# Kernel optimization log

Hardware: AMD Instinct MI355X
Metric: run time of the kernel (lower is better)

The kernel has to match this reference:

```python
import jax, jax.numpy as jnp
import numpy as np

N, DIN, DOUT = 8192, 128, 128
NEG = -9.0e15  # the module's -9000000000000000.0 mask value
ALPHA = 0.2    # LeakyReLU negative slope


def setup_inputs() -> dict:
    key = jax.random.key(0)
    kx, ka, kw, ks, kr = jax.random.split(key, 5)
    X = jax.random.normal(kx, (N, DIN), dtype=jnp.float32)
    A = (jax.random.uniform(ka, (N, N)) < 0.01).astype(jnp.float32)
    A = A.at[jnp.arange(N), jnp.arange(N)].set(1.0)
    # Linear weight (Kaiming-uniform-ish range is irrelevant to math; use Xavier)
    lim_w = float(np.sqrt(6.0 / (DIN + DOUT)))
    W = jax.random.uniform(kw, (DOUT, DIN), jnp.float32, -lim_w, lim_w)
    b = jnp.zeros((DOUT,), jnp.float32)
    lim_a = float(np.sqrt(6.0 / (DOUT + 1)))
    a_s = jax.random.uniform(ks, (DOUT, 1), jnp.float32, -lim_a, lim_a)
    a_r = jax.random.uniform(kr, (DOUT, 1), jnp.float32, -lim_a, lim_a)
    return {"X": X, "A": A, "W": W, "b": b, "a_s": a_s, "a_r": a_r}


def reference(X, A, W, b, a_s, a_r):
    # H_in = Linear(X)
    H = X @ W.T + b                         # [N, DOUT]
    s = H @ a_s                             # [N, 1] source scores
    r = H @ a_r                             # [N, 1] receiver scores
    # M_s = A * s (broadcast over cols), M_r = A * r^T (broadcast over rows)
    e = jax.nn.leaky_relu(A * s + A * r.T, negative_slope=ALPHA)  # [N, N]
    masked = jnp.where(A > 0, e, NEG)
    att = jax.nn.softmax(masked, axis=1)    # row-stochastic attention
    H_out = att @ H                         # [N, DOUT]  (act = Identity, dropout = eval)
    # NOTE: the torch module applies LayerNorm into a local var but returns
    # the pre-norm H_out, so LayerNorm is dead code. A and [] passthroughs omitted.
    return H_out
```

## Files before the change

### kernel.cpp

```cpp
#include <hip/hip_runtime.h>

#define N 8192
#define D 128
#define ALPHA 0.2f
#define RCAP 256

__global__ __launch_bounds__(256) void linear_kernel(
    const float* __restrict__ X, const float* __restrict__ W,
    const float* __restrict__ b, const float* __restrict__ a_s,
    const float* __restrict__ a_r,
    float* __restrict__ H, float* __restrict__ sv, float* __restrict__ rv)
{
    __shared__ float Xs[128 * 36];
    __shared__ float Ws[64 * 132];

    const int tid = threadIdx.x;
    const int i0  = blockIdx.x * 32;

    for (int idx = tid; idx < 32 * 128; idx += 256) {
        const int row = idx >> 7, k = idx & 127;
        Xs[k * 36 + row] = X[(i0 + row) * D + k];
    }

    float acc[4][4] = {};
    const int ty = tid >> 5, tx = tid & 31;
    const int rbase = ty * 4, cbase = tx * 4;

    for (int kb = 0; kb < 2; ++kb) {
        __syncthreads();
        for (int idx = tid; idx < 64 * 128; idx += 256) {
            const int o = idx >> 6, kk = idx & 63;
            Ws[kk * 132 + o] = W[o * D + kb * 64 + kk];
        }
        __syncthreads();
        #pragma unroll
        for (int kk = 0; kk < 64; ++kk) {
            const float4 xv = *(const float4*)&Xs[(kb * 64 + kk) * 36 + rbase];
            const float4 wv = *(const float4*)&Ws[kk * 132 + cbase];
            const float xr[4] = {xv.x, xv.y, xv.z, xv.w};
            const float wc[4] = {wv.x, wv.y, wv.z, wv.w};
            #pragma unroll
            for (int r = 0; r < 4; ++r)
                #pragma unroll
                for (int c = 0; c < 4; ++c)
                    acc[r][c] += xr[r] * wc[c];
        }
    }

    const float4 bv  = *(const float4*)&b[cbase];
    const float4 asv = *(const float4*)&a_s[cbase];
    const float4 arv = *(const float4*)&a_r[cbase];
    #pragma unroll
    for (int r = 0; r < 4; ++r) {
        float4 h;
        h.x = acc[r][0] + bv.x;
        h.y = acc[r][1] + bv.y;
        h.z = acc[r][2] + bv.z;
        h.w = acc[r][3] + bv.w;
        *(float4*)&H[(size_t)(i0 + rbase + r) * D + cbase] = h;
        float ps = h.x * asv.x + h.y * asv.y + h.z * asv.z + h.w * asv.w;
        float pr = h.x * arv.x + h.y * arv.y + h.z * arv.z + h.w * arv.w;
        #pragma unroll
        for (int off = 16; off > 0; off >>= 1) {
            ps += __shfl_xor(ps, off);
            pr += __shfl_xor(pr, off);
        }
        if (tx == 0) {
            sv[i0 + rbase + r] = ps;
            rv[i0 + rbase + r] = pr;
        }
    }
}

__global__ __launch_bounds__(256, 6) void attn_fused(
    const float* __restrict__ A, const float* __restrict__ H,
    const float* __restrict__ sv, const float* __restrict__ rv,
    float* __restrict__ out)
{
    __shared__ float2 s_l[4][RCAP];

    const int wave = threadIdx.x >> 6;
    const int lane = threadIdx.x & 63;
    const int i    = blockIdx.x * 4 + wave;

    const float4* __restrict__ Arow = (const float4*)(A + (size_t)i * N);

    float4 buf[2][4];
    #pragma unroll
    for (int q = 0; q < 4; ++q) buf[0][q] = Arow[q * 64 + lane];

    int cnt = 0;
    #pragma unroll 1
    for (int it = 0; it < 8; ++it) {
        const int cb = it & 1;
        if (it < 7) {
            #pragma unroll
            for (int q = 0; q < 4; ++q)
                buf[cb ^ 1][q] = Arow[(it + 1) * 256 + q * 64 + lane];
        }
        unsigned m = 0;
        #pragma unroll
        for (int q = 0; q < 4; ++q) {
            const float4 a = buf[cb][q];
            m |= (a.x != 0.0f ? 1u : 0u) << (q * 4 + 0);
            m |= (a.y != 0.0f ? 1u : 0u) << (q * 4 + 1);
            m |= (a.z != 0.0f ? 1u : 0u) << (q * 4 + 2);
            m |= (a.w != 0.0f ? 1u : 0u) << (q * 4 + 3);
        }
        const int c = __popc(m);
        int scan = c;
        #pragma unroll
        for (int off = 1; off < 64; off <<= 1) {
            const int t = __shfl_up(scan, off);
            if (lane >= off) scan += t;
        }
        int base = cnt + scan - c;
        cnt += __shfl(scan, 63);
        while (m) {
            const int k = __ffs(m) - 1;
            m &= m - 1;
            const int q = k >> 2, e = k & 3;
            if (base < RCAP)
                s_l[wave][base].y = __int_as_float(it * 1024 + q * 256 + lane * 4 + e);
            ++base;
        }
    }
    cnt = (cnt < RCAP) ? cnt : RCAP;

    const float si = sv[i];
    float zv[4];
    #pragma unroll
    for (int k = 0; k < 4; ++k) {
        const int p = lane + 64 * k;
        const bool act = (p < cnt);
        const int j = act ? __float_as_int(s_l[wave][p].y) : 0;
        float z = si + rv[j];
        z = (z > 0.0f) ? z : ALPHA * z;
        zv[k] = act ? z : -3.0e38f;
    }
    float lm = fmaxf(fmaxf(zv[0], zv[1]), fmaxf(zv[2], zv[3]));
    #pragma unroll
    for (int off = 32; off > 0; off >>= 1) lm = fmaxf(lm, __shfl_xor(lm, off));

    float sl = 0.0f;
    float wv4[4];
    #pragma unroll
    for (int k = 0; k < 4; ++k) {
        const int p = lane + 64 * k;
        const float w = (p < cnt) ? __expf(zv[k] - lm) : 0.0f;
        wv4[k] = w;
        sl += w;
    }
    #pragma unroll
    for (int off = 32; off > 0; off >>= 1) sl += __shfl_xor(sl, off);
    const float inv = 1.0f / sl;

    #pragma unroll
    for (int k = 0; k < 4; ++k) {
        const int p = lane + 64 * k;
        if (p < cnt) s_l[wave][p].x = wv4[k] * inv;
    }

    float2 acc = make_float2(0.0f, 0.0f);
    const float* __restrict__ Hl = H + 2 * lane;
    #pragma unroll 4
    for (int p = 0; p < cnt; ++p) {
        const float2 wj = s_l[wave][p];
        const int   j  = __float_as_int(wj.y);
        const float2 h = *(const float2*)&Hl[(size_t)j * D];
        acc.x += wj.x * h.x;
        acc.y += wj.x * h.y;
    }
    *(float2*)&out[(size_t)i * D + 2 * lane] = acc;
}

extern "C" void kernel_launch(void* const* d_in, const int* in_sizes, int n_in,
                              void* d_out, int out_size, void* d_ws, size_t ws_size,
                              hipStream_t stream) {
    const float* X   = (const float*)d_in[0];
    const float* A   = (const float*)d_in[1];
    const float* W   = (const float*)d_in[2];
    const float* b   = (const float*)d_in[3];
    const float* a_s = (const float*)d_in[4];
    const float* a_r = (const float*)d_in[5];
    float* out = (float*)d_out;

    float* H  = (float*)d_ws;
    float* sv = H + (size_t)N * D;
    float* rv = sv + N;

    linear_kernel<<<256, 256, 0, stream>>>(X, W, b, a_s, a_r, H, sv, rv);
    attn_fused<<<N / 4, 256, 0, stream>>>(A, H, sv, rv, out);
}
```

Measured before the change: 446.7 us.

## Split adjacency scan into separate bitmask kernel and gather kernel

Moves the dense adjacency read into a dedicated streaming kernel that packs each row into 16-bit masks, then a second kernel reads the compact masks to build neighbor lists, compute softmax, and gather H. The aim is to let the bandwidth-bound A scan run without the gather's registers and dependent loads, and to shrink the per-row scan to a single prefix pass. The cost is an extra launch plus writing and reading an 8 MB mask buffer in workspace, and the ordering of columns is reconstructed through index arithmetic.

```diff
diff --git a/kernel.cpp b/kernel.cpp
--- a/kernel.cpp
+++ b/kernel.cpp
@@ -72,8 +72,45 @@
     }
 }
 
-__global__ __launch_bounds__(256, 6) void attn_fused(
-    const float* __restrict__ A, const float* __restrict__ H,
+__global__ __launch_bounds__(256) void mask_kernel(
+    const float* __restrict__ A, unsigned short* __restrict__ Mk)
+{
+    const int wave = threadIdx.x >> 6;
+    const int lane = threadIdx.x & 63;
+    const int row  = blockIdx.x * 4 + wave;
+
+    const float4* __restrict__ Arow = (const float4*)(A + (size_t)row * N);
+    unsigned short* __restrict__ Mrow = Mk + (size_t)row * 512;
+
+    #pragma unroll 2
+    for (int it = 0; it < 8; ++it) {
+        const float4 a0 = Arow[it * 256 +   0 + lane];
+        const float4 a1 = Arow[it * 256 +  64 + lane];
+        const float4 a2 = Arow[it * 256 + 128 + lane];
+        const float4 a3 = Arow[it * 256 + 192 + lane];
+        unsigned m = 0;
+        m |= (a0.x != 0.0f ? 1u : 0u) << 0;
+        m |= (a0.y != 0.0f ? 1u : 0u) << 1;
+        m |= (a0.z != 0.0f ? 1u : 0u) << 2;
+        m |= (a0.w != 0.0f ? 1u : 0u) << 3;
+        m |= (a1.x != 0.0f ? 1u : 0u) << 4;
+        m |= (a1.y != 0.0f ? 1u : 0u) << 5;
+        m |= (a1.z != 0.0f ? 1u : 0u) << 6;
+        m |= (a1.w != 0.0f ? 1u : 0u) << 7;
+        m |= (a2.x != 0.0f ? 1u : 0u) << 8;
+        m |= (a2.y != 0.0f ? 1u : 0u) << 9;
+        m |= (a2.z != 0.0f ? 1u : 0u) << 10;
+        m |= (a2.w != 0.0f ? 1u : 0u) << 11;
+        m |= (a3.x != 0.0f ? 1u : 0u) << 12;
+        m |= (a3.y != 0.0f ? 1u : 0u) << 13;
+        m |= (a3.z != 0.0f ? 1u : 0u) << 14;
+        m |= (a3.w != 0.0f ? 1u : 0u) << 15;
+        Mrow[it * 64 + lane] = (unsigned short)m;
+    }
+}
+
+__global__ __launch_bounds__(256, 8) void gather_kernel(
+    const unsigned short* __restrict__ Mk, const float* __restrict__ H,
     const float* __restrict__ sv, const float* __restrict__ rv,
     float* __restrict__ out)
 {
@@ -83,49 +120,34 @@
     const int lane = threadIdx.x & 63;
     const int i    = blockIdx.x * 4 + wave;
 
-    const float4* __restrict__ Arow = (const float4*)(A + (size_t)i * N);
-
-    float4 buf[2][4];
-    #pragma unroll
-    for (int q = 0; q < 4; ++q) buf[0][q] = Arow[q * 64 + lane];
-
-    int cnt = 0;
-    #pragma unroll 1
-    for (int it = 0; it < 8; ++it) {
-        const int cb = it & 1;
-        if (it < 7) {
-            #pragma unroll
-            for (int q = 0; q < 4; ++q)
-                buf[cb ^ 1][q] = Arow[(it + 1) * 256 + q * 64 + lane];
-        }
-        unsigned m = 0;
-        #pragma unroll
-        for (int q = 0; q < 4; ++q) {
-            const float4 a = buf[cb][q];
-            m |= (a.x != 0.0f ? 1u : 0u) << (q * 4 + 0);
-            m |= (a.y != 0.0f ? 1u : 0u) << (q * 4 + 1);
-            m |= (a.z != 0.0f ? 1u : 0u) << (q * 4 + 2);
-            m |= (a.w != 0.0f ? 1u : 0u) << (q * 4 + 3);
-        }
-        const int c = __popc(m);
-        int scan = c;
-        #pragma unroll
-        for (int off = 1; off < 64; off <<= 1) {
-            const int t = __shfl_up(scan, off);
-            if (lane >= off) scan += t;
-        }
-        int base = cnt + scan - c;
-        cnt += __shfl(scan, 63);
-        while (m) {
-            const int k = __ffs(m) - 1;
-            m &= m - 1;
-            const int q = k >> 2, e = k & 3;
-            if (base < RCAP)
-                s_l[wave][base].y = __int_as_float(it * 1024 + q * 256 + lane * 4 + e);
+    const uint4 mw = ((const uint4*)(Mk + (size_t)i * 512))[lane];
+    unsigned wv[4] = {mw.x, mw.y, mw.z, mw.w};
+
+    const int c = __popc(wv[0]) + __popc(wv[1]) + __popc(wv[2]) + __popc(wv[3]);
+
+    int scan = c;
+    #pragma unroll
+    for (int off = 1; off < 64; off <<= 1) {
+        const int t = __shfl_up(scan, off);
+        if (lane >= off) scan += t;
+    }
+    int base = scan - c;
+    int cnt  = __shfl(scan, 63);
+    cnt = (cnt < RCAP) ? cnt : RCAP;
+
+    #pragma unroll
+    for (int widx = 0; widx < 4; ++widx) {
+        unsigned mm = wv[widx];
+        while (mm) {
+            const int p = __ffs(mm) - 1;
+            mm &= mm - 1;
+            const int k = lane * 8 + widx * 2 + (p >> 4);
+            const int b = p & 15;
+            const int col = ((k >> 6) << 10) + ((b >> 2) << 8) + ((k & 63) << 2) + (b & 3);
+            if (base < RCAP) s_l[wave][base].y = __int_as_float(col);
             ++base;
         }
     }
-    cnt = (cnt < RCAP) ? cnt : RCAP;
 
     const float si = sv[i];
     float zv[4];
@@ -188,7 +210,9 @@
     float* H  = (float*)d_ws;
     float* sv = H + (size_t)N * D;
     float* rv = sv + N;
+    unsigned short* Mk = (unsigned short*)(rv + N);
 
     linear_kernel<<<256, 256, 0, stream>>>(X, W, b, a_s, a_r, H, sv, rv);
-    attn_fused<<<N / 4, 256, 0, stream>>>(A, H, sv, rv, out);
-}
+    mask_kernel<<<N / 4, 256, 0, stream>>>(A, Mk);
+    gather_kernel<<<N / 4, 256, 0, stream>>>(Mk, H, sv, rv, out);
+}
```

Measured after the change: 411.9 us. 1.08x faster.

## Process one adjacency row per block with all four waves cooperating

Applied to the files above, without the earlier changes.

The attention kernel now gives each block a single row instead of one row per wave. The four waves each scan a quarter of the row at once, using nontemporal vector loads with no serial double-buffered loop, and combine their offsets through shared memory. Softmax reductions and the weighted gather of H are spread over 256 threads with float4 loads and a cross-wave partial-sum reduction. This raises memory-level parallelism on the dense A stream and shortens the gather per row, at the cost of several block barriers and four times as many blocks.

```diff
diff --git a/kernel.cpp b/kernel.cpp
--- a/kernel.cpp
+++ b/kernel.cpp
@@ -4,6 +4,8 @@
 #define D 128
 #define ALPHA 0.2f
 #define RCAP 256
+
+typedef float fx4 __attribute__((ext_vector_type(4)));
 
 __global__ __launch_bounds__(256) void linear_kernel(
     const float* __restrict__ X, const float* __restrict__ W,
@@ -72,106 +74,115 @@
     }
 }
 
-__global__ __launch_bounds__(256, 6) void attn_fused(
+__global__ __launch_bounds__(256) void attn_fused(
     const float* __restrict__ A, const float* __restrict__ H,
     const float* __restrict__ sv, const float* __restrict__ rv,
     float* __restrict__ out)
 {
-    __shared__ float2 s_l[4][RCAP];
-
-    const int wave = threadIdx.x >> 6;
-    const int lane = threadIdx.x & 63;
-    const int i    = blockIdx.x * 4 + wave;
-
-    const float4* __restrict__ Arow = (const float4*)(A + (size_t)i * N);
-
-    float4 buf[2][4];
-    #pragma unroll
-    for (int q = 0; q < 4; ++q) buf[0][q] = Arow[q * 64 + lane];
-
-    int cnt = 0;
-    #pragma unroll 1
-    for (int it = 0; it < 8; ++it) {
-        const int cb = it & 1;
-        if (it < 7) {
-            #pragma unroll
-            for (int q = 0; q < 4; ++q)
-                buf[cb ^ 1][q] = Arow[(it + 1) * 256 + q * 64 + lane];
-        }
-        unsigned m = 0;
-        #pragma unroll
-        for (int q = 0; q < 4; ++q) {
-            const float4 a = buf[cb][q];
-            m |= (a.x != 0.0f ? 1u : 0u) << (q * 4 + 0);
-            m |= (a.y != 0.0f ? 1u : 0u) << (q * 4 + 1);
-            m |= (a.z != 0.0f ? 1u : 0u) << (q * 4 + 2);
-            m |= (a.w != 0.0f ? 1u : 0u) << (q * 4 + 3);
-        }
-        const int c = __popc(m);
-        int scan = c;
-        #pragma unroll
-        for (int off = 1; off < 64; off <<= 1) {
-            const int t = __shfl_up(scan, off);
-            if (lane >= off) scan += t;
-        }
-        int base = cnt + scan - c;
-        cnt += __shfl(scan, 63);
-        while (m) {
-            const int k = __ffs(m) - 1;
-            m &= m - 1;
-            const int q = k >> 2, e = k & 3;
-            if (base < RCAP)
-                s_l[wave][base].y = __int_as_float(it * 1024 + q * 256 + lane * 4 + e);
+    __shared__ float2 s_l[RCAP];
+    __shared__ int    s_wcnt[4];
+    __shared__ float  s_red[8];
+    __shared__ float4 s_part[4][32];
+
+    const int tid  = threadIdx.x;
+    const int wave = tid >> 6;
+    const int lane = tid & 63;
+    const int i    = blockIdx.x;
+
+    const fx4* __restrict__ Arow = (const fx4*)(A + (size_t)i * N);
+
+    unsigned m = 0;
+    #pragma unroll
+    for (int q = 0; q < 8; ++q) {
+        const fx4 a = __builtin_nontemporal_load(&Arow[wave * 512 + q * 64 + lane]);
+        m |= (a.x != 0.0f ? 1u : 0u) << (q * 4 + 0);
+        m |= (a.y != 0.0f ? 1u : 0u) << (q * 4 + 1);
+        m |= (a.z != 0.0f ? 1u : 0u) << (q * 4 + 2);
+        m |= (a.w != 0.0f ? 1u : 0u) << (q * 4 + 3);
+    }
+
+    const int c = __popc(m);
+    int scan = c;
+    #pragma unroll
+    for (int off = 1; off < 64; off <<= 1) {
+        const int t = __shfl_up(scan, off);
+        if (lane >= off) scan += t;
+    }
+    if (lane == 63) s_wcnt[wave] = scan;
+    __syncthreads();
+    int base = scan - c;
+    #pragma unroll
+    for (int w2 = 0; w2 < 4; ++w2)
+        if (w2 < wave) base += s_wcnt[w2];
+    int cnt = s_wcnt[0] + s_wcnt[1] + s_wcnt[2] + s_wcnt[3];
+    cnt = (cnt < RCAP) ? cnt : RCAP;
+
+    {
+        unsigned mm = m;
+        while (mm) {
+            const int p = __ffs(mm) - 1;
+            mm &= mm - 1;
+            const int col = wave * 2048 + ((p >> 2) << 8) + (lane << 2) + (p & 3);
+            if (base < RCAP) s_l[base].y = __int_as_float(col);
             ++base;
         }
     }
-    cnt = (cnt < RCAP) ? cnt : RCAP;
+    __syncthreads();
 
     const float si = sv[i];
-    float zv[4];
-    #pragma unroll
-    for (int k = 0; k < 4; ++k) {
-        const int p = lane + 64 * k;
-        const bool act = (p < cnt);
-        const int j = act ? __float_as_int(s_l[wave][p].y) : 0;
-        float z = si + rv[j];
+    float z = -3.0e38f;
+    if (tid < cnt) {
+        const int j = __float_as_int(s_l[tid].y);
+        z = si + rv[j];
         z = (z > 0.0f) ? z : ALPHA * z;
-        zv[k] = act ? z : -3.0e38f;
-    }
-    float lm = fmaxf(fmaxf(zv[0], zv[1]), fmaxf(zv[2], zv[3]));
+    }
+    float lm = z;
     #pragma unroll
     for (int off = 32; off > 0; off >>= 1) lm = fmaxf(lm, __shfl_xor(lm, off));
-
-    float sl = 0.0f;
-    float wv4[4];
-    #pragma unroll
-    for (int k = 0; k < 4; ++k) {
-        const int p = lane + 64 * k;
-        const float w = (p < cnt) ? __expf(zv[k] - lm) : 0.0f;
-        wv4[k] = w;
-        sl += w;
-    }
+    if (lane == 0) s_red[wave] = lm;
+    __syncthreads();
+    const float M = fmaxf(fmaxf(s_red[0], s_red[1]), fmaxf(s_red[2], s_red[3]));
+
+    const float w = (tid < cnt) ? __expf(z - M) : 0.0f;
+    float sl = w;
     #pragma unroll
     for (int off = 32; off > 0; off >>= 1) sl += __shfl_xor(sl, off);
-    const float inv = 1.0f / sl;
-
-    #pragma unroll
-    for (int k = 0; k < 4; ++k) {
-        const int p = lane + 64 * k;
-        if (p < cnt) s_l[wave][p].x = wv4[k] * inv;
-    }
-
-    float2 acc = make_float2(0.0f, 0.0f);
-    const float* __restrict__ Hl = H + 2 * lane;
+    if (lane == 0) s_red[4 + wave] = sl;
+    __syncthreads();
+    const float inv = 1.0f / (s_red[4] + s_red[5] + s_red[6] + s_red[7]);
+    if (tid < cnt) s_l[tid].x = w * inv;
+    __syncthreads();
+
+    const int hw = tid >> 5;
+    const int fs = tid & 31;
+    float4 acc = make_float4(0.0f, 0.0f, 0.0f, 0.0f);
     #pragma unroll 4
-    for (int p = 0; p < cnt; ++p) {
-        const float2 wj = s_l[wave][p];
+    for (int p = hw; p < cnt; p += 8) {
+        const float2 wj = s_l[p];
         const int   j  = __float_as_int(wj.y);
-        const float2 h = *(const float2*)&Hl[(size_t)j * D];
+        const float4 h = *(const float4*)&H[(size_t)j * D + fs * 4];
         acc.x += wj.x * h.x;
         acc.y += wj.x * h.y;
-    }
-    *(float2*)&out[(size_t)i * D + 2 * lane] = acc;
+        acc.z += wj.x * h.z;
+        acc.w += wj.x * h.w;
+    }
+    acc.x += __shfl_xor(acc.x, 32);
+    acc.y += __shfl_xor(acc.y, 32);
+    acc.z += __shfl_xor(acc.z, 32);
+    acc.w += __shfl_xor(acc.w, 32);
+    if ((lane >> 5) == 0) s_part[wave][fs] = acc;
+    __syncthreads();
+    if (tid < 32) {
+        float4 v = s_part[0][tid];
+        const float4 v1 = s_part[1][tid];
+        const float4 v2 = s_part[2][tid];
+        const float4 v3 = s_part[3][tid];
+        v.x += v1.x + v2.x + v3.x;
+        v.y += v1.y + v2.y + v3.y;
+        v.z += v1.z + v2.z + v3.z;
+        v.w += v1.w + v2.w + v3.w;
+        *(float4*)&out[(size_t)i * D + tid * 4] = v;
+    }
 }
 
 extern "C" void kernel_launch(void* const* d_in, const int* in_sizes, int n_in,
@@ -190,5 +201,5 @@
     float* rv = sv + N;
 
     linear_kernel<<<256, 256, 0, stream>>>(X, W, b, a_s, a_r, H, sv, rv);
-    attn_fused<<<N / 4, 256, 0, stream>>>(A, H, sv, rv, out);
+    attn_fused<<<N, 256, 0, stream>>>(A, H, sv, rv, out);
 }
```

After: 374.1 us. 1.19x faster.
